# Kernel tuning notes

Hardware: AMD Instinct MI355X
Metric: run time of the kernel (lower is better)

The kernel has to match this reference:

```python
import jax, jax.numpy as jnp
import numpy as np

B, T, C, H, K = 16, 8192, 256, 256, 7


def setup_inputs() -> dict:
    key = jax.random.key(0)
    ks = jax.random.split(key, 6)
    x = jax.random.normal(ks[0], (B, T, C), dtype=jnp.float32)
    # ragged lengths in [T//2, T]; padding_mask: True = padding (at tail)
    lengths = jax.random.randint(ks[1], (B,), T // 2, T + 1)
    padding_mask = jnp.arange(T)[None, :] >= lengths[:, None]
    w1 = jax.random.normal(ks[2], (H, C, K), dtype=jnp.float32) / np.sqrt(C * K)
    b1 = jnp.zeros((H,), jnp.float32)
    w2 = jax.random.normal(ks[3], (H, H, 3), dtype=jnp.float32) / np.sqrt(H * 3)
    b2 = jnp.zeros((H,), jnp.float32)
    w3 = jax.random.normal(ks[4], (2, H, 1), dtype=jnp.float32) / np.sqrt(H)
    b3 = jnp.zeros((2,), jnp.float32)
    return {"x": x, "padding_mask": padding_mask,
            "w1": w1, "b1": b1, "w2": w2, "b2": b2, "w3": w3, "b3": b3}


def _conv1d(h, w, b, pad):
    # h: (B, Cin, T), w: (Cout, Cin, K) torch OIW layout
    y = jax.lax.conv_general_dilated(h, w, (1,), [(pad, pad)],
                                     dimension_numbers=("NCH", "OIH", "NCH"))
    return y + b[None, :, None]


def _boundary_logits(x, w1, b1, w2, b2, w3, b3):
    # RebornSegmenter.forward (dropout is identity in eval)
    h = jnp.transpose(x, (0, 2, 1))            # (B, C, T)
    h = jax.nn.relu(_conv1d(h, w1, b1, K // 2))
    h = jax.nn.relu(_conv1d(h, w2, b2, 1))
    h = _conv1d(h, w3, b3, 0)                  # (B, 2, T)
    return jnp.transpose(h, (0, 2, 1))         # (B, T, 2)


def _segment_pool(xb, sid):
    # xb: (T, C), sid: (T,) in [0, T] (T == dropped/padding)
    sums = jax.ops.segment_sum(xb, sid, num_segments=T)
    cnt = jax.ops.segment_sum(jnp.ones((T,), xb.dtype), sid, num_segments=T)
    return sums, cnt


def reference(x, padding_mask, w1, b1, w2, b2, w3, b3):
    # pre_segment with deterministic=True (boundary = argmax of conv logits)
    boundary_logits = _boundary_logits(x, w1, b1, w2, b2, w3, b3)
    boundary = jnp.argmax(boundary_logits, axis=-1)            # (B, T)
    is_b = (boundary == 1) & (~padding_mask)
    # token t belongs to segment = number of boundaries in [0..t]
    seg_id = jnp.cumsum(is_b.astype(jnp.int32), axis=1)
    seg_id = jnp.where(padding_mask, T, seg_id)  # out-of-range -> dropped
    sums, cnt = jax.vmap(_segment_pool)(x, seg_id)             # (B,T,C),(B,T)
    # segment mean; empty segments -> 0 (output padded to T segments, jit-safe;
    # torch crops to max segment count, extra columns here are flagged padded)
    new_logits = jnp.where(cnt[..., None] > 0,
                           sums / jnp.maximum(cnt, 1.0)[..., None], 0.0)
    nb = jnp.sum(is_b, axis=1)
    n_valid = jnp.where(jnp.any(~padding_mask, axis=1), nb + 1, 0)
    new_pad = jnp.arange(T)[None, :] >= n_valid[:, None]       # (B, T)
    return new_logits, new_pad
```

## Files before the change

kernel.cpp:

```cpp
#include <hip/hip_runtime.h>
#include <cstdint>
#include <cstddef>

#define BSZ 16
#define T   8192
#define CDIM 256
#define HDIM 256
#define KW  7

constexpr int BT = BSZ * T;
constexpr float TAU = 2e-3f;
constexpr int RCAP = 8192;

typedef __attribute__((ext_vector_type(8))) short short8;
typedef _Float16 half8 __attribute__((ext_vector_type(8)));
typedef __attribute__((ext_vector_type(4))) float f32x4;

constexpr size_t B_W1T  = 0;
constexpr size_t B_W2T  = B_W1T + 1835008;
constexpr size_t B_V    = B_W2T + 786432;
constexpr size_t B_D    = B_V + 1024;
constexpr size_t B_ISB  = B_D + 524288;
constexpr size_t B_SID  = B_ISB + 524288;
constexpr size_t B_SST  = B_SID + 524288;
constexpr size_t B_SEN  = B_SST + 524288;
constexpr size_t B_NV   = B_SEN + 524288;
constexpr size_t B_UCT  = B_NV + 64;
constexpr size_t B_UL   = B_UCT + 16;
constexpr size_t B_ZERO = B_UL + 32768;
constexpr size_t B_W1B  = B_ZERO + 256;
constexpr size_t B_W2B  = B_W1B + 917504;
constexpr size_t B_H1F  = B_W2B + 393216;
constexpr size_t B_DSUM = B_H1F + 25165824;

__device__ __forceinline__ void gl_lds16(const void* g, void* l) {
    __builtin_amdgcn_global_load_lds(
        (const __attribute__((address_space(1))) unsigned int*)g,
        (__attribute__((address_space(3))) unsigned int*)l,
        16, 0, 0);
}

__device__ __forceinline__ unsigned short f16_rne(float f) {
    _Float16 h = (_Float16)f;
    return __builtin_bit_cast(unsigned short, h);
}

__global__ void repack_kernel(const float* __restrict__ w1, const float* __restrict__ w2,
                              const float* __restrict__ w3,
                              float* __restrict__ W1R, float* __restrict__ W2R,
                              float* __restrict__ v,
                              unsigned short* __restrict__ W1b, unsigned short* __restrict__ W2b)
{
    int idx = blockIdx.x * blockDim.x + threadIdx.x;
    int stride = gridDim.x * blockDim.x;
    for (int i = idx; i < HDIM * 1792; i += stride) {
        int h = i / 1792, kc = i % 1792, kw = kc >> 8, c = kc & 255;
        float wv = w1[(size_t)h * 1792 + c * 7 + kw];
        W1R[i] = wv;
        W1b[i] = f16_rne(wv);
    }
    for (int i = idx; i < HDIM * 768; i += stride) {
        int h = i / 768, kc = i % 768, kw = kc >> 8, c = kc & 255;
        float wv = w2[(size_t)h * 768 + c * 3 + kw];
        W2R[i] = wv;
        W2b[i] = f16_rne(wv);
    }
    if (idx < HDIM) v[idx] = w3[HDIM + idx] - w3[idx];
}

__global__ __launch_bounds__(256) void xcast_kernel(const float* __restrict__ x,
                                                    unsigned short* __restrict__ xhf)
{
    size_t i = ((size_t)blockIdx.x * 256 + threadIdx.x) * 8;
    float4 a = *(const float4*)(x + i);
    float4 b = *(const float4*)(x + i + 4);
    short8 o;
    o[0] = (short)f16_rne(a.x); o[1] = (short)f16_rne(a.y);
    o[2] = (short)f16_rne(a.z); o[3] = (short)f16_rne(a.w);
    o[4] = (short)f16_rne(b.x); o[5] = (short)f16_rne(b.y);
    o[6] = (short)f16_rne(b.z); o[7] = (short)f16_rne(b.w);
    *(short8*)(xhf + i) = o;
}

__global__ __launch_bounds__(256) void conv1_mfma(
    const unsigned short* __restrict__ xhf,
    const unsigned short* __restrict__ Wb,
    const float* __restrict__ b1,
    const unsigned short* __restrict__ zerobuf,
    unsigned short* __restrict__ h1)
{
    __shared__ half8 A8[4 * 322];
    __shared__ half8 B8[16 * 130];
    const int tid = threadIdx.x, lane = tid & 63, wid = tid >> 6;
    const int b  = blockIdx.x >> 5;
    const int t0 = (blockIdx.x & 31) << 8;
    const int h0 = blockIdx.y << 7;
    const int q = lane >> 4, l15 = lane & 15;
    const unsigned short* xb = xhf + (size_t)b * T * 256;

    f32x4 acc[4][8] = {};

    for (int cc = 0; cc < 8; ++cc) {
        const int c0 = cc << 5;
        __syncthreads();
        #pragma unroll
        for (int part = 0; part < 5; ++part) {
            int row = part * 64 + lane;
            int t = t0 + row - 3;
            const unsigned short* src = (row < 262 && t >= 0 && t < T)
                ? xb + (size_t)t * 256 + c0 + wid * 8 : zerobuf;
            gl_lds16(src, &A8[wid * 322 + part * 64]);
        }
        #pragma unroll
        for (int s = 0; s < 8; ++s) {
            int bq = s >> 1, half = s & 1;
            const unsigned short* src = Wb + (size_t)(h0 + half * 64 + lane) * 1792
                                        + wid * 256 + c0 + bq * 8;
            gl_lds16(src, &B8[(wid * 4 + bq) * 130 + half * 64]);
        }
        __syncthreads();
        #pragma unroll
        for (int kw = 0; kw < 4; ++kw) {
            half8 ah[4], bh[8];
            const int rbase = wid * 64 + l15 + kw;
            #pragma unroll
            for (int i = 0; i < 4; ++i) ah[i] = A8[q * 322 + rbase + i * 16];
            #pragma unroll
            for (int j = 0; j < 8; ++j) bh[j] = B8[(kw * 4 + q) * 130 + j * 16 + l15];
            #pragma unroll
            for (int i = 0; i < 4; ++i)
                #pragma unroll
                for (int j = 0; j < 8; ++j)
                    acc[i][j] = __builtin_amdgcn_mfma_f32_16x16x32_f16(ah[i], bh[j], acc[i][j], 0, 0, 0);
        }
        __syncthreads();
        #pragma unroll
        for (int s = 0; s < 6; ++s) {
            int seg = wid * 6 + s;
            int kw2 = seg >> 3, bq = (seg >> 1) & 3, half = seg & 1;
            const unsigned short* src = Wb + (size_t)(h0 + half * 64 + lane) * 1792
                                        + (kw2 + 4) * 256 + c0 + bq * 8;
            gl_lds16(src, &B8[(kw2 * 4 + bq) * 130 + half * 64]);
        }
        __syncthreads();
        #pragma unroll
        for (int kw = 4; kw < 7; ++kw) {
            half8 ah[4], bh[8];
            const int rbase = wid * 64 + l15 + kw;
            const int slot = kw - 4;
            #pragma unroll
            for (int i = 0; i < 4; ++i) ah[i] = A8[q * 322 + rbase + i * 16];
            #pragma unroll
            for (int j = 0; j < 8; ++j) bh[j] = B8[(slot * 4 + q) * 130 + j * 16 + l15];
            #pragma unroll
            for (int i = 0; i < 4; ++i)
                #pragma unroll
                for (int j = 0; j < 8; ++j)
                    acc[i][j] = __builtin_amdgcn_mfma_f32_16x16x32_f16(ah[i], bh[j], acc[i][j], 0, 0, 0);
        }
    }
    #pragma unroll
    for (int j = 0; j < 8; ++j) {
        int h = h0 + j * 16 + l15;
        float bb = b1[h];
        #pragma unroll
        for (int i = 0; i < 4; ++i) {
            int tb = t0 + wid * 64 + i * 16 + q * 4;
            #pragma unroll
            for (int r = 0; r < 4; ++r)
                h1[(size_t)(b * T + tb + r) * 256 + h] = f16_rne(fmaxf(acc[i][j][r] + bb, 0.f));
        }
    }
}

__global__ __launch_bounds__(256) void conv2_mfma(
    const unsigned short* __restrict__ h1,
    const unsigned short* __restrict__ Wb,
    const float* __restrict__ b2, const float* __restrict__ v,
    const unsigned short* __restrict__ zerobuf,
    float* __restrict__ dlog)
{
    __shared__ half8 A8[4 * 322];
    __shared__ half8 B8[12 * 130];
    const int tid = threadIdx.x, lane = tid & 63, wid = tid >> 6;
    const int b  = blockIdx.x >> 5;
    const int t0 = (blockIdx.x & 31) << 8;
    const int h0 = blockIdx.y << 7;
    const int q = lane >> 4, l15 = lane & 15;
    const unsigned short* hb = h1 + (size_t)b * T * 256;

    f32x4 acc[4][8] = {};

    for (int cc = 0; cc < 8; ++cc) {
        const int c0 = cc << 5;
        __syncthreads();
        #pragma unroll
        for (int part = 0; part < 5; ++part) {
            int row = part * 64 + lane;
            int t = t0 + row - 1;
            const unsigned short* src = (row < 258 && t >= 0 && t < T)
                ? hb + (size_t)t * 256 + c0 + wid * 8 : zerobuf;
            gl_lds16(src, &A8[wid * 322 + part * 64]);
        }
        #pragma unroll
        for (int s = 0; s < 6; ++s) {
            int seg = wid * 6 + s;
            int kw = seg >> 3, bq = (seg >> 1) & 3, half = seg & 1;
            const unsigned short* src = Wb + (size_t)(h0 + half * 64 + lane) * 768
                                        + kw * 256 + c0 + bq * 8;
            gl_lds16(src, &B8[(kw * 4 + bq) * 130 + half * 64]);
        }
        __syncthreads();
        #pragma unroll
        for (int kw = 0; kw < 3; ++kw) {
            half8 ah[4], bh[8];
            const int rbase = wid * 64 + l15 + kw;
            #pragma unroll
            for (int i = 0; i < 4; ++i) ah[i] = A8[q * 322 + rbase + i * 16];
            #pragma unroll
            for (int j = 0; j < 8; ++j) bh[j] = B8[(kw * 4 + q) * 130 + j * 16 + l15];
            #pragma unroll
            for (int i = 0; i < 4; ++i)
                #pragma unroll
                for (int j = 0; j < 8; ++j)
                    acc[i][j] = __builtin_amdgcn_mfma_f32_16x16x32_f16(ah[i], bh[j], acc[i][j], 0, 0, 0);
        }
    }
    float vv[8], bb[8];
    #pragma unroll
    for (int j = 0; j < 8; ++j) {
        int h = h0 + j * 16 + l15;
        vv[j] = v[h]; bb[j] = b2[h];
    }
    #pragma unroll
    for (int i = 0; i < 4; ++i) {
        int tb = t0 + wid * 64 + i * 16 + q * 4;
        #pragma unroll
        for (int r = 0; r < 4; ++r) {
            float s = 0.f;
            #pragma unroll
            for (int j = 0; j < 8; ++j)
                s += fmaxf(acc[i][j][r] + bb[j], 0.f) * vv[j];
            #pragma unroll
            for (int m = 1; m < 16; m <<= 1)
                s += __shfl_xor(s, m, 64);
            if (l15 == 0) atomicAdd(&dlog[b * T + tb + r], s);
        }
    }
}

__global__ void boundary_kernel(const float* __restrict__ d, const int* __restrict__ padmask,
                                const float* __restrict__ b3,
                                int* __restrict__ isb, int* __restrict__ ucount,
                                int* __restrict__ ulist)
{
    int bt = blockIdx.x * 256 + threadIdx.x;
    if (bt >= BT) return;
    int pad = padmask[bt];
    float dd = d[bt] + (b3[1] - b3[0]);
    isb[bt] = (pad == 0 && dd > 0.f) ? 1 : 0;
    if (pad == 0 && fabsf(dd) < TAU) {
        int slot = atomicAdd(ucount, 1);
        if (slot < RCAP) ulist[slot] = bt;
    }
}

__global__ __launch_bounds__(256) void recheck_h1(
    const float* __restrict__ x, const float* __restrict__ W1R,
    const float* __restrict__ b1, const float* __restrict__ zerof,
    const int* __restrict__ ulist, const int* __restrict__ ucount,
    float* __restrict__ h1f)
{
    __shared__ float xs[9 * CDIM];
    int n = *ucount; if (n > RCAP) n = RCAP;
    const int tid = threadIdx.x, lane = tid & 63, wid = tid >> 6;
    const int g = tid >> 4, l = tid & 15;
    const int nit = 4 * n;
    for (int item = blockIdx.x; item < nit; item += gridDim.x) {
        const int li = item >> 2, hc = item & 3;
        const int bt = ulist[li];
        const int b = bt >> 13, t = bt & (T - 1);
        __syncthreads();
        for (int r = wid; r < 9; r += 4) {
            int tt = t + r - 4;
            const float* src = (tt >= 0 && tt < T)
                ? x + (size_t)(b * T + tt) * CDIM + lane * 4 : zerof;
            gl_lds16(src, &xs[r * CDIM]);
        }
        __syncthreads();
        #pragma unroll
        for (int s = 0; s < 4; ++s) {
            const int h = hc * 64 + s * 16 + g;
            const float* wr = &W1R[(size_t)h * 1792];
            double p0 = 0.0, p1 = 0.0, p2 = 0.0;
            #pragma unroll 7
            for (int it = 0; it < 28; ++it) {
                const int e = it * 64 + l * 4;
                float4 w4 = *(const float4*)&wr[e];
                double w0 = (double)w4.x, w1v = (double)w4.y,
                       w2v = (double)w4.z, w3v = (double)w4.w;
                const float* x0 = &xs[e];
                p0 += w0 * (double)x0[0] + w1v * (double)x0[1]
                    + w2v * (double)x0[2] + w3v * (double)x0[3];
                const float* x1 = &xs[256 + e];
                p1 += w0 * (double)x1[0] + w1v * (double)x1[1]
                    + w2v * (double)x1[2] + w3v * (double)x1[3];
                const float* x2 = &xs[512 + e];
                p2 += w0 * (double)x2[0] + w1v * (double)x2[1]
                    + w2v * (double)x2[2] + w3v * (double)x2[3];
            }
            #pragma unroll
            for (int m = 1; m < 16; m <<= 1) {
                p0 += __shfl_xor(p0, m);
                p1 += __shfl_xor(p1, m);
                p2 += __shfl_xor(p2, m);
            }
            if (l == 0) {
                double bb = (double)b1[h];
                double a0 = bb + p0, a1 = bb + p1, a2 = bb + p2;
                float* o = &h1f[(size_t)li * 768];
                o[0 * 256 + h] = (t - 1 >= 0 && a0 > 0.0) ? (float)a0 : 0.f;
                o[1 * 256 + h] = (a1 > 0.0) ? (float)a1 : 0.f;
                o[2 * 256 + h] = (t + 1 < T && a2 > 0.0) ? (float)a2 : 0.f;
            }
        }
    }
}

__global__ __launch_bounds__(256) void recheck_h2(
    const float* __restrict__ h1f, const float* __restrict__ W2R,
    const float* __restrict__ b2, const float* __restrict__ w3,
    const int* __restrict__ ulist, const int* __restrict__ ucount,
    double* __restrict__ dsum)
{
    __shared__ float hs[768];
    __shared__ double red[64];
    int n = *ucount; if (n > RCAP) n = RCAP;
    const int tid = threadIdx.x, lane = tid & 63, wid = tid >> 6;
    const int g = tid >> 4, l = tid & 15;
    const int nit = 4 * n;
    for (int item = blockIdx.x; item < nit; item += gridDim.x) {
        const int li = item >> 2, hc = item & 3;
        __syncthreads();
        if (wid < 3)
            gl_lds16(h1f + (size_t)li * 768 + wid * 256 + lane * 4, &hs[wid * 256]);
        __syncthreads();
        #pragma unroll
        for (int s = 0; s < 4; ++s) {
            const int h = hc * 64 + s * 16 + g;
            const float* wr = &W2R[(size_t)h * 768];
            double c0 = 0.0;
            #pragma unroll
            for (int it = 0; it < 12; ++it) {
                const int e = it * 64 + l * 4;
                float4 w4 = *(const float4*)&wr[e];
                const float* hv = &hs[e];
                c0 += (double)w4.x * (double)hv[0] + (double)w4.y * (double)hv[1]
                    + (double)w4.z * (double)hv[2] + (double)w4.w * (double)hv[3];
            }
            #pragma unroll
            for (int m = 1; m < 16; m <<= 1) c0 += __shfl_xor(c0, m);
            if (l == 0) {
                double acc2 = (double)b2[h] + c0;
                double h2v = acc2 > 0.0 ? acc2 : 0.0;
                double vd = (double)w3[HDIM + h] - (double)w3[h];
                red[s * 16 + g] = vd * h2v;
            }
        }
        __syncthreads();
        if (tid < 32) red[tid] += red[tid + 32];
        __syncthreads();
        if (tid < 16) red[tid] += red[tid + 16];
        __syncthreads();
        if (tid == 0) {
            double ssum = 0.0;
            #pragma unroll
            for (int i = 0; i < 16; ++i) ssum += red[i];
            atomicAdd(&dsum[li], ssum);
        }
    }
}

__global__ void recheck_final(const double* __restrict__ dsum, const float* __restrict__ b3,
                              const int* __restrict__ ulist, const int* __restrict__ ucount,
                              int* __restrict__ isb)
{
    int n = *ucount; if (n > RCAP) n = RCAP;
    int li = blockIdx.x * 256 + threadIdx.x;
    if (li >= n) return;
    double dd = dsum[li] + ((double)b3[1] - (double)b3[0]);
    isb[ulist[li]] = (dd > 0.0) ? 1 : 0;
}

__global__ __launch_bounds__(1024) void scan_kernel(
    const int* __restrict__ isb, const int* __restrict__ padmask,
    int* __restrict__ sid, int* __restrict__ nvalid)
{
    __shared__ int ssum[1024];
    const int b = blockIdx.x, tid = threadIdx.x;
    const int base = b * T;
    int vals[8]; int s = 0;
    #pragma unroll
    for (int i = 0; i < 8; ++i) { vals[i] = isb[base + tid * 8 + i]; s += vals[i]; }
    ssum[tid] = s;
    __syncthreads();
    for (int off = 1; off < 1024; off <<= 1) {
        int add = (tid >= off) ? ssum[tid - off] : 0;
        __syncthreads();
        ssum[tid] += add;
        __syncthreads();
    }
    int run = ssum[tid] - s;
    #pragma unroll
    for (int i = 0; i < 8; ++i) {
        int t = tid * 8 + i;
        run += vals[i];
        sid[base + t] = (padmask[base + t] != 0) ? T : run;
    }
    if (tid == 1023) {
        int nb = ssum[1023];
        nvalid[b] = (padmask[base] == 0) ? (nb + 1) : 0;
    }
}

__global__ void segbounds_kernel(const int* __restrict__ sid, const int* __restrict__ padmask,
                                 int* __restrict__ sst, int* __restrict__ sen)
{
    int bt = blockIdx.x * 256 + threadIdx.x;
    if (bt >= BT) return;
    if (padmask[bt] != 0) return;
    int t = bt & (T - 1);
    int b = bt >> 13;
    int s = sid[bt];
    if (t == 0) {
        if (s < T) sst[b * T + s] = 0;
    } else if (s != sid[bt - 1]) {
        if (s < T) sst[b * T + s] = t;
    }
    bool last = (t == T - 1) || (padmask[bt + 1] != 0);
    if (s < T && (last || sid[bt + 1] != s)) sen[b * T + s] = t + 1;
}

__global__ __launch_bounds__(256) void pool_kernel(
    const float* __restrict__ x, const int* __restrict__ sst,
    const int* __restrict__ sen, const int* __restrict__ nvalid,
    float* __restrict__ out)
{
    int slot = blockIdx.x * 4 + (threadIdx.x >> 6);
    int lane = threadIdx.x & 63;
    int b = slot >> 13;
    int s = slot & (T - 1);
    int nv = nvalid[b];
    float4 res = make_float4(0.f, 0.f, 0.f, 0.f);
    if (s < nv) {
        int st = sst[slot], en = sen[slot];
        if (st >= 0 && en > st) {
            float4 a = make_float4(0.f, 0.f, 0.f, 0.f);
            const float* xp = &x[(size_t)(b * T + st) * CDIM + lane * 4];
            for (int t = st; t < en; ++t) {
                float4 xv = *(const float4*)xp;
                a.x += xv.x; a.y += xv.y; a.z += xv.z; a.w += xv.w;
                xp += CDIM;
            }
            float inv = 1.f / (float)(en - st);
            res = make_float4(a.x * inv, a.y * inv, a.z * inv, a.w * inv);
        }
    }
    *(float4*)&out[(size_t)slot * CDIM + lane * 4] = res;
    if (lane == 0) out[(size_t)BT * CDIM + slot] = (s < nv) ? 0.f : 1.f;
}

extern "C" void kernel_launch(void* const* d_in, const int* in_sizes, int n_in,
                              void* d_out, int out_size, void* d_ws, size_t ws_size,
                              hipStream_t stream)
{
    const float* x  = (const float*)d_in[0];
    const int* padmask = (const int*)d_in[1];
    const float* w1 = (const float*)d_in[2];
    const float* b1 = (const float*)d_in[3];
    const float* w2 = (const float*)d_in[4];
    const float* b2 = (const float*)d_in[5];
    const float* w3 = (const float*)d_in[6];
    const float* b3 = (const float*)d_in[7];

    char* ws = (char*)d_ws;
    float* W1R = (float*)(ws + B_W1T);
    float* W2R = (float*)(ws + B_W2T);
    float* v   = (float*)(ws + B_V);
    float* dlog = (float*)(ws + B_D);
    int* isb = (int*)(ws + B_ISB);
    int* sid = (int*)(ws + B_SID);
    int* sst = (int*)(ws + B_SST);
    int* sen = (int*)(ws + B_SEN);
    int* nv  = (int*)(ws + B_NV);
    int* uct = (int*)(ws + B_UCT);
    int* ul  = (int*)(ws + B_UL);
    unsigned short* zerobuf = (unsigned short*)(ws + B_ZERO);
    unsigned short* W1b = (unsigned short*)(ws + B_W1B);
    unsigned short* W2b = (unsigned short*)(ws + B_W2B);
    float* h1f = (float*)(ws + B_H1F);
    double* dsum = (double*)(ws + B_DSUM);

    float* out = (float*)d_out;
    unsigned short* h1  = (unsigned short*)out;
    unsigned short* xhf = h1 + (size_t)BT * 256;

    hipMemsetAsync(dlog, 0, BT * sizeof(float), stream);
    hipMemsetAsync(sst, 0xFF, BT * sizeof(int), stream);
    hipMemsetAsync(sen, 0xFF, BT * sizeof(int), stream);
    hipMemsetAsync(uct, 0, sizeof(int), stream);
    hipMemsetAsync(zerobuf, 0, 256, stream);
    hipMemsetAsync(dsum, 0, RCAP * sizeof(double), stream);

    repack_kernel<<<1024, 256, 0, stream>>>(w1, w2, w3, W1R, W2R, v, W1b, W2b);
    xcast_kernel<<<BT * 256 / (8 * 256), 256, 0, stream>>>(x, xhf);
    conv1_mfma<<<dim3(BSZ * (T / 256), HDIM / 128), 256, 0, stream>>>(
        xhf, W1b, b1, zerobuf, h1);
    conv2_mfma<<<dim3(BSZ * (T / 256), HDIM / 128), 256, 0, stream>>>(
        h1, W2b, b2, v, zerobuf, dlog);
    boundary_kernel<<<BT / 256, 256, 0, stream>>>(dlog, padmask, b3, isb, uct, ul);
    recheck_h1<<<4096, 256, 0, stream>>>(x, W1R, b1, (const float*)zerobuf, ul, uct, h1f);
    recheck_h2<<<4096, 256, 0, stream>>>(h1f, W2R, b2, w3, ul, uct, dsum);
    recheck_final<<<RCAP / 256, 256, 0, stream>>>(dsum, b3, ul, uct, isb);
    scan_kernel<<<BSZ, 1024, 0, stream>>>(isb, padmask, sid, nv);
    segbounds_kernel<<<BT / 256, 256, 0, stream>>>(sid, padmask, sst, sen);
    pool_kernel<<<BT / 4, 256, 0, stream>>>(x, sst, sen, nv, out);
}
```

Before: 710.2 us.

## Double-buffer LDS tiles in conv1 and conv2 MFMA kernels

Both convolution kernels now keep two LDS buffers for the input and weight tiles. The next channel chunk is prefetched into one buffer while MFMAs run on the other. Conv1 also stages all seven weight taps at once, which removes its mid-loop reload and extra barriers. The aim is to hide global-to-LDS load latency behind compute. In exchange, conv1's LDS footprint grows to roughly 157KB, which limits each CU to one block. The gain also depends on whether the compiler's waitcnt placement stalls on the async LDS loads before the compute phase.

```diff
diff --git a/kernel.cpp b/kernel.cpp
--- a/kernel.cpp
+++ b/kernel.cpp
@@ -82,6 +82,32 @@
     *(short8*)(xhf + i) = o;
 }
 
+__device__ __forceinline__ void c1_stageA(const unsigned short* xb, const unsigned short* zerobuf,
+                                          half8* Ab, int t0, int c0, int lane, int wid)
+{
+    #pragma unroll
+    for (int part = 0; part < 5; ++part) {
+        int row = part * 64 + lane;
+        int t = t0 + row - 3;
+        const unsigned short* src = (row < 262 && t >= 0 && t < T)
+            ? xb + (size_t)t * 256 + c0 + wid * 8 : zerobuf;
+        gl_lds16(src, &Ab[wid * 322 + part * 64]);
+    }
+}
+__device__ __forceinline__ void c1_stageB(const unsigned short* Wb, half8* Bb,
+                                          int h0, int c0, int lane, int wid)
+{
+    #pragma unroll
+    for (int s = 0; s < 14; ++s) {
+        int bs = wid * 14 + s;
+        int slot = bs >> 1, half = bs & 1;
+        int kw = slot >> 2, bq = slot & 3;
+        const unsigned short* src = Wb + (size_t)(h0 + half * 64 + lane) * 1792
+                                    + kw * 256 + c0 + bq * 8;
+        gl_lds16(src, &Bb[slot * 130 + half * 64]);
+    }
+}
+
 __global__ __launch_bounds__(256) void conv1_mfma(
     const unsigned short* __restrict__ xhf,
     const unsigned short* __restrict__ Wb,
@@ -89,8 +115,8 @@
     const unsigned short* __restrict__ zerobuf,
     unsigned short* __restrict__ h1)
 {
-    __shared__ half8 A8[4 * 322];
-    __shared__ half8 B8[16 * 130];
+    __shared__ half8 A8[2][4 * 322];
+    __shared__ half8 B8[2][28 * 130];
     const int tid = threadIdx.x, lane = tid & 63, wid = tid >> 6;
     const int b  = blockIdx.x >> 5;
     const int t0 = (blockIdx.x & 31) << 8;
@@ -100,58 +126,25 @@
 
     f32x4 acc[4][8] = {};
 
+    c1_stageA(xb, zerobuf, A8[0], t0, 0, lane, wid);
+    c1_stageB(Wb, B8[0], h0, 0, lane, wid);
+
     for (int cc = 0; cc < 8; ++cc) {
-        const int c0 = cc << 5;
-        __syncthreads();
+        const int cur = cc & 1;
+        __syncthreads();
+        if (cc < 7) {
+            const int c1 = (cc + 1) << 5;
+            c1_stageA(xb, zerobuf, A8[cur ^ 1], t0, c1, lane, wid);
+            c1_stageB(Wb, B8[cur ^ 1], h0, c1, lane, wid);
+        }
         #pragma unroll
-        for (int part = 0; part < 5; ++part) {
-            int row = part * 64 + lane;
-            int t = t0 + row - 3;
-            const unsigned short* src = (row < 262 && t >= 0 && t < T)
-                ? xb + (size_t)t * 256 + c0 + wid * 8 : zerobuf;
-            gl_lds16(src, &A8[wid * 322 + part * 64]);
-        }
-        #pragma unroll
-        for (int s = 0; s < 8; ++s) {
-            int bq = s >> 1, half = s & 1;
-            const unsigned short* src = Wb + (size_t)(h0 + half * 64 + lane) * 1792
-                                        + wid * 256 + c0 + bq * 8;
-            gl_lds16(src, &B8[(wid * 4 + bq) * 130 + half * 64]);
-        }
-        __syncthreads();
-        #pragma unroll
-        for (int kw = 0; kw < 4; ++kw) {
+        for (int kw = 0; kw < 7; ++kw) {
             half8 ah[4], bh[8];
             const int rbase = wid * 64 + l15 + kw;
             #pragma unroll
-            for (int i = 0; i < 4; ++i) ah[i] = A8[q * 322 + rbase + i * 16];
-            #pragma unroll
-            for (int j = 0; j < 8; ++j) bh[j] = B8[(kw * 4 + q) * 130 + j * 16 + l15];
-            #pragma unroll
-            for (int i = 0; i < 4; ++i)
-                #pragma unroll
-                for (int j = 0; j < 8; ++j)
-                    acc[i][j] = __builtin_amdgcn_mfma_f32_16x16x32_f16(ah[i], bh[j], acc[i][j], 0, 0, 0);
-        }
-        __syncthreads();
-        #pragma unroll
-        for (int s = 0; s < 6; ++s) {
-            int seg = wid * 6 + s;
-            int kw2 = seg >> 3, bq = (seg >> 1) & 3, half = seg & 1;
-            const unsigned short* src = Wb + (size_t)(h0 + half * 64 + lane) * 1792
-                                        + (kw2 + 4) * 256 + c0 + bq * 8;
-            gl_lds16(src, &B8[(kw2 * 4 + bq) * 130 + half * 64]);
-        }
-        __syncthreads();
-        #pragma unroll
-        for (int kw = 4; kw < 7; ++kw) {
-            half8 ah[4], bh[8];
-            const int rbase = wid * 64 + l15 + kw;
-            const int slot = kw - 4;
-            #pragma unroll
-            for (int i = 0; i < 4; ++i) ah[i] = A8[q * 322 + rbase + i * 16];
-            #pragma unroll
-            for (int j = 0; j < 8; ++j) bh[j] = B8[(slot * 4 + q) * 130 + j * 16 + l15];
+            for (int i = 0; i < 4; ++i) ah[i] = A8[cur][q * 322 + rbase + i * 16];
+            #pragma unroll
+            for (int j = 0; j < 8; ++j) bh[j] = B8[cur][(kw * 4 + q) * 130 + j * 16 + l15];
             #pragma unroll
             for (int i = 0; i < 4; ++i)
                 #pragma unroll
@@ -173,6 +166,32 @@
     }
 }
 
+__device__ __forceinline__ void c2_stageA(const unsigned short* hb, const unsigned short* zerobuf,
+                                          half8* Ab, int t0, int c0, int lane, int wid)
+{
+    #pragma unroll
+    for (int part = 0; part < 5; ++part) {
+        int row = part * 64 + lane;
+        int t = t0 + row - 1;
+        const unsigned short* src = (row < 258 && t >= 0 && t < T)
+            ? hb + (size_t)t * 256 + c0 + wid * 8 : zerobuf;
+        gl_lds16(src, &Ab[wid * 322 + part * 64]);
+    }
+}
+__device__ __forceinline__ void c2_stageB(const unsigned short* Wb, half8* Bb,
+                                          int h0, int c0, int lane, int wid)
+{
+    #pragma unroll
+    for (int s = 0; s < 6; ++s) {
+        int bs = wid * 6 + s;
+        int slot = bs >> 1, half = bs & 1;
+        int kw = slot >> 2, bq = slot & 3;
+        const unsigned short* src = Wb + (size_t)(h0 + half * 64 + lane) * 768
+                                    + kw * 256 + c0 + bq * 8;
+        gl_lds16(src, &Bb[slot * 130 + half * 64]);
+    }
+}
+
 __global__ __launch_bounds__(256) void conv2_mfma(
     const unsigned short* __restrict__ h1,
     const unsigned short* __restrict__ Wb,
@@ -180,8 +199,8 @@
     const unsigned short* __restrict__ zerobuf,
     float* __restrict__ dlog)
 {
-    __shared__ half8 A8[4 * 322];
-    __shared__ half8 B8[12 * 130];
+    __shared__ half8 A8[2][4 * 322];
+    __shared__ half8 B8[2][12 * 130];
     const int tid = threadIdx.x, lane = tid & 63, wid = tid >> 6;
     const int b  = blockIdx.x >> 5;
     const int t0 = (blockIdx.x & 31) << 8;
@@ -191,34 +210,25 @@
 
     f32x4 acc[4][8] = {};
 
+    c2_stageA(hb, zerobuf, A8[0], t0, 0, lane, wid);
+    c2_stageB(Wb, B8[0], h0, 0, lane, wid);
+
     for (int cc = 0; cc < 8; ++cc) {
-        const int c0 = cc << 5;
-        __syncthreads();
-        #pragma unroll
-        for (int part = 0; part < 5; ++part) {
-            int row = part * 64 + lane;
-            int t = t0 + row - 1;
-            const unsigned short* src = (row < 258 && t >= 0 && t < T)
-                ? hb + (size_t)t * 256 + c0 + wid * 8 : zerobuf;
-            gl_lds16(src, &A8[wid * 322 + part * 64]);
-        }
-        #pragma unroll
-        for (int s = 0; s < 6; ++s) {
-            int seg = wid * 6 + s;
-            int kw = seg >> 3, bq = (seg >> 1) & 3, half = seg & 1;
-            const unsigned short* src = Wb + (size_t)(h0 + half * 64 + lane) * 768
-                                        + kw * 256 + c0 + bq * 8;
-            gl_lds16(src, &B8[(kw * 4 + bq) * 130 + half * 64]);
-        }
-        __syncthreads();
+        const int cur = cc & 1;
+        __syncthreads();
+        if (cc < 7) {
+            const int c1 = (cc + 1) << 5;
+            c2_stageA(hb, zerobuf, A8[cur ^ 1], t0, c1, lane, wid);
+            c2_stageB(Wb, B8[cur ^ 1], h0, c1, lane, wid);
+        }
         #pragma unroll
         for (int kw = 0; kw < 3; ++kw) {
             half8 ah[4], bh[8];
             const int rbase = wid * 64 + l15 + kw;
             #pragma unroll
-            for (int i = 0; i < 4; ++i) ah[i] = A8[q * 322 + rbase + i * 16];
-            #pragma unroll
-            for (int j = 0; j < 8; ++j) bh[j] = B8[(kw * 4 + q) * 130 + j * 16 + l15];
+            for (int i = 0; i < 4; ++i) ah[i] = A8[cur][q * 322 + rbase + i * 16];
+            #pragma unroll
+            for (int j = 0; j < 8; ++j) bh[j] = B8[cur][(kw * 4 + q) * 130 + j * 16 + l15];
             #pragma unroll
             for (int i = 0; i < 4; ++i)
                 #pragma unroll
```

After: 708.0 us. No clear change (-0.3%).
